# Optimization experiments

Measured on AMD Instinct MI355X. Metric: run time of the kernel, lower is better.

The kernel has to match this reference:

```python
import jax, jax.numpy as jnp
import numpy as np

B, N, D_MODEL, N_HEADS, WINDOW = 2, 2048, 1024, 16, 512
HEAD_DIM = D_MODEL // N_HEADS

def setup_inputs() -> dict:
    key = jax.random.key(0)
    k1, k2, k3 = jax.random.split(key, 3)
    x = jax.random.normal(k1, (B, N, D_MODEL), dtype=jnp.float32)
    W_qkv = jax.random.normal(k2, (D_MODEL, 3 * D_MODEL), dtype=jnp.float32) * 0.02
    W_proj = jax.random.normal(k3, (D_MODEL, D_MODEL), dtype=jnp.float32) * 0.02
    b_proj = jnp.zeros((D_MODEL,), dtype=jnp.float32)
    return {"x": x, "W_qkv": W_qkv, "W_proj": W_proj, "b_proj": b_proj}

def reference(x, W_qkv, W_proj, b_proj):
    Bx, Nx, C = x.shape
    H, Dh = N_HEADS, C // N_HEADS
    scale = Dh ** -0.5
    window = min(WINDOW, Nx)
    half = window // 2
    # qkv: [B,N,3C] -> [3,B,H,N,Dh]
    qkv = (x @ W_qkv).reshape(Bx, Nx, 3, H, Dh).transpose(2, 0, 3, 1, 4)
    q, k, v = qkv[0], qkv[1], qkv[2]
    # banded mask: allowed iff i-half <= j <= i+half
    i = jnp.arange(Nx)[:, None]
    j = jnp.arange(Nx)[None, :]
    allowed = jnp.abs(i - j) <= half  # [N,N] bool
    attn = jnp.einsum('bhqd,bhkd->bhqk', q, k) * scale
    attn = jnp.where(allowed[None, None], attn, -jnp.inf)
    attn = jax.nn.softmax(attn, axis=-1)
    out = jnp.einsum('bhqk,bhkd->bhqd', attn, v)
    out = out.transpose(0, 2, 1, 3).reshape(Bx, Nx, C)
    return out @ W_proj + b_proj
```

## Files before the change

kernel.cpp:

```cpp
#include <hip/hip_runtime.h>
#include <stdint.h>


typedef _Float16 f16x8 __attribute__((ext_vector_type(8)));
typedef _Float16 f16x4 __attribute__((ext_vector_type(4)));
typedef __fp16   fp16x2n __attribute__((ext_vector_type(2)));
typedef float    f32x4 __attribute__((ext_vector_type(4)));
typedef float    f32x16 __attribute__((ext_vector_type(16)));

#define MFMA16(a, b, c) __builtin_amdgcn_mfma_f32_16x16x32_f16((a), (b), (c), 0, 0, 0)
#define MFMA32(a, b, c) __builtin_amdgcn_mfma_f32_32x32x16_f16((a), (b), (c), 0, 0, 0)

__device__ __forceinline__ void gload16(const void* g, void* l) {
  __builtin_amdgcn_global_load_lds(
      (const __attribute__((address_space(1))) void*)g,
      (__attribute__((address_space(3))) void*)l, 16, 0, 0);
}

__device__ __forceinline__ unsigned pk2(float a, float b) {
  fp16x2n t = __builtin_amdgcn_cvt_pkrtz(a, b);
  return __builtin_bit_cast(unsigned, t);
}

__global__ __launch_bounds__(256) void prep(const float* __restrict__ x,
                                            const float* __restrict__ wqkv,
                                            const float* __restrict__ wproj,
                                            _Float16* __restrict__ Xb,
                                            _Float16* __restrict__ Wqt,
                                            _Float16* __restrict__ Wpt) {
  __shared__ float t[64][65];
  const int id = blockIdx.x, tid = threadIdx.x;
  if (id < 4096) {
    int i = (id * 256 + tid) * 4;
    float4 v = *(const float4*)(x + i);
    f16x4 h;
    h[0] = (_Float16)v.x; h[1] = (_Float16)v.y;
    h[2] = (_Float16)v.z; h[3] = (_Float16)v.w;
    *(f16x4*)(Xb + i) = h;
    return;
  }
  const float* in; _Float16* out; int N, bx, by;
  if (id < 4864) { int tt = id - 4096; in = wqkv; out = Wqt; N = 3072; bx = tt % 48; by = tt / 48; }
  else           { int tt = id - 4864; in = wproj; out = Wpt; N = 1024; bx = tt & 15; by = tt >> 4; }
  const int n0 = bx * 64, k0 = by * 64;
  {
    int j = tid & 63;
#pragma unroll
    for (int p = 0; p < 16; p++) {
      int i = p * 4 + (tid >> 6);
      t[i][j] = in[(size_t)(k0 + i) * N + n0 + j];
    }
  }
  __syncthreads();
  {
    int i = tid & 63;
#pragma unroll
    for (int p = 0; p < 16; p++) {
      int j = p * 4 + (tid >> 6);
      out[(size_t)(n0 + j) * 1024 + k0 + i] = (_Float16)t[i][j];
    }
  }
}

__global__ __launch_bounds__(256) void vtrans(const _Float16* __restrict__ V,
                                              _Float16* __restrict__ Vt) {
  __shared__ _Float16 t[64][66];
  const int tid = threadIdx.x;
  const int bh = blockIdx.y, n0 = blockIdx.x * 64;
  const _Float16* Vg = V + (size_t)bh * 131072;
  {
    int dh0 = (tid & 7) * 8;
#pragma unroll
    for (int p = 0; p < 2; p++) {
      int nl = p * 32 + (tid >> 3);
      f16x8 v = *(const f16x8*)(Vg + (size_t)(n0 + nl) * 64 + dh0);
#pragma unroll
      for (int e = 0; e < 8; e++) t[nl][dh0 + e] = v[e];
    }
  }
  __syncthreads();
  {
    int dh = tid >> 2, nb = (tid & 3) * 16;
    f16x8 a, b;
#pragma unroll
    for (int e = 0; e < 8; e++) { a[e] = t[nb + e][dh]; b[e] = t[nb + 8 + e][dh]; }
    _Float16* dst = Vt + (size_t)bh * 131072 + (size_t)dh * 2048 + n0 + nb;
    *(f16x8*)dst = a;
    *(f16x8*)(dst + 8) = b;
  }
}

template <int BM, int BN, int EPI>
__global__ __launch_bounds__(256) void gemm16(const _Float16* __restrict__ A,
                                              const _Float16* __restrict__ Bt,
                                              const int K,
                                              _Float16* __restrict__ oh,
                                              float* __restrict__ of,
                                              const float* __restrict__ bias,
                                              const int Nout) {
  constexpr int RF = BM / 32, CF = BN / 32;
  constexpr int SLABS = (BM + BN) / 8;
  __shared__ __align__(16) char smem[(BM + BN) * 128];
  char* As = smem;
  char* Bs = smem + BM * 128;
  const int tid = threadIdx.x, wave = tid >> 6, lane = tid & 63;
  const int il = lane & 15, ih = lane >> 4;
  const int bm = blockIdx.y * BM, bn = blockIdx.x * BN;
  const int wm = wave >> 1, wn = wave & 1;
  const int rs = lane >> 3, cp = lane & 7;

  f32x4 acc[RF][CF] = {};

  for (int k0 = 0; k0 < K; k0 += 64) {
    __syncthreads();
#pragma unroll
    for (int s0 = 0; s0 < SLABS / 4; s0++) {
      int s = wave + s0 * 4;
      int row = s * 8 + rs;
      int c = cp ^ (row & 7);
      if (row < BM)
        gload16(A + (size_t)(bm + row) * K + k0 + c * 8, As + s * 1024);
      else
        gload16(Bt + (size_t)(bn + row - BM) * K + k0 + c * 8, smem + s * 1024);
    }
    __syncthreads();
#pragma unroll
    for (int ks = 0; ks < 2; ks++) {
      f16x8 af[RF], bf[CF];
#pragma unroll
      for (int rf = 0; rf < RF; rf++) {
        int R = wm * (BM / 2) + rf * 16 + il;
        af[rf] = *(const f16x8*)(As + R * 128 + (((ks * 4 + ih) ^ (R & 7)) * 16));
      }
#pragma unroll
      for (int cf = 0; cf < CF; cf++) {
        int C = wn * (BN / 2) + cf * 16 + il;
        bf[cf] = *(const f16x8*)(Bs + C * 128 + (((ks * 4 + ih) ^ (C & 7)) * 16));
      }
#pragma unroll
      for (int rf = 0; rf < RF; rf++)
#pragma unroll
        for (int cf = 0; cf < CF; cf++)
          acc[rf][cf] = MFMA16(af[rf], bf[cf], acc[rf][cf]);
    }
  }

#pragma unroll
  for (int rf = 0; rf < RF; rf++)
#pragma unroll
    for (int cf = 0; cf < CF; cf++)
#pragma unroll
      for (int r = 0; r < 4; r++) {
        int row = bm + wm * (BM / 2) + rf * 16 + ih * 4 + r;
        int col = bn + wn * (BN / 2) + cf * 16 + il;
        float v = acc[rf][cf][r];
        if (EPI == 0) {
          int sec = col >> 10, cc = col & 1023;
          if (sec == 0) v *= 0.18033688f;
          size_t plane = (size_t)(sec * 32 + (row >> 11) * 16 + (cc >> 6));
          oh[plane * 131072 + (size_t)(row & 2047) * 64 + (cc & 63)] = (_Float16)v;
        } else {
          of[(size_t)row * Nout + col] = v + bias[col];
        }
      }
}

__global__ __launch_bounds__(512) void attn(const _Float16* __restrict__ QKV,
                                            const _Float16* __restrict__ VT,
                                            _Float16* __restrict__ O2) {
  __shared__ __align__(16) char smem[65536];
  char* Qs = smem;
  const int tid = threadIdx.x, wave = tid >> 6, lane = tid & 63;
  const int cl = lane & 31, hl = lane >> 5;
  const int rs = lane >> 3, cp = lane & 7;
  const int q0 = blockIdx.x * 256, bh = blockIdx.y;
  const _Float16* Qg = QKV + (size_t)bh * 131072;
  const _Float16* Kg = QKV + 4194304 + (size_t)bh * 131072;
  const _Float16* Vg = VT + (size_t)bh * 131072;
  const int t0 = (q0 >= 256) ? q0 - 256 : 0;
  const int t1 = (q0 + 512 <= 2048) ? q0 + 512 : 2048;
  const int niter = (t1 - t0) >> 6;

#pragma unroll
  for (int s0 = 0; s0 < 4; s0++) {
    int s = wave * 4 + s0;
    int row = s * 8 + rs;
    int c = cp ^ (row & 7);
    gload16(Qg + (size_t)(q0 + row) * 64 + c * 8, Qs + s * 1024);
  }
  {
    char* B0 = smem + 32768;
    int row = wave * 8 + rs;
    int c = cp ^ (row & 7);
    gload16(Kg + (size_t)(t0 + row) * 64 + c * 8, B0 + wave * 1024);
    gload16(Vg + (size_t)row * 2048 + t0 + c * 8, B0 + 8192 + wave * 1024);
  }
  __syncthreads();

  f16x8 bq[4];
  {
    int row = 32 * wave + cl;
#pragma unroll
    for (int ks = 0; ks < 4; ks++)
      bq[ks] = *(const f16x8*)(Qs + row * 128 + (((ks * 2 + hl) ^ (row & 7)) * 16));
  }

  f32x16 oacc[2] = {};
  float l_acc = 0.f;
  const int a0 = q0 + 32 * wave;

  for (int i = 0; i < niter; i++) {
    const int kt = t0 + i * 64;
    char* Bc = smem + 32768 + (i & 1) * 16384;
    if (i + 1 < niter) {
      char* Bn = smem + 32768 + ((i + 1) & 1) * 16384;
      int row = wave * 8 + rs;
      int c = cp ^ (row & 7);
      gload16(Kg + (size_t)(kt + 64 + row) * 64 + c * 8, Bn + wave * 1024);
      gload16(Vg + (size_t)row * 2048 + (kt + 64) + c * 8, Bn + 8192 + wave * 1024);
    }
    char* Ksm = Bc;
    char* Vsm = Bc + 8192;
#pragma unroll
    for (int cb = 0; cb < 2; cb++) {
      const int d0 = a0 - (kt + 32 * cb);
      if (d0 >= 288 || d0 <= -288) continue;
      f32x16 st = {};
#pragma unroll
      for (int ks = 0; ks < 4; ks++) {
        int krow = 32 * cb + cl;
        f16x8 ak = *(const f16x8*)(Ksm + krow * 128 + (((ks * 2 + hl) ^ (krow & 7)) * 16));
        st = MFMA32(ak, bq[ks], st);
      }
      uint32_t q4x[4], q4y[4];
#pragma unroll
      for (int g = 0; g < 4; g++) {
        float v[4];
#pragma unroll
        for (int i2 = 0; i2 < 4; i2++) {
          float e = __builtin_amdgcn_exp2f(st[4 * g + i2]);
          int kl = 8 * g + 4 * hl + i2;
          if (d0 == 256) e = (cl <= kl) ? e : 0.f;
          else if (d0 == -256) e = (cl >= kl) ? e : 0.f;
          l_acc += e;
          v[i2] = e;
        }
        q4x[g] = pk2(v[0], v[1]);
        q4y[g] = pk2(v[2], v[3]);
      }
#pragma unroll
      for (int ks2 = 0; ks2 < 2; ks2++) {
        uint32_t qax = q4x[2 * ks2], qay = q4y[2 * ks2];
        uint32_t qbx = q4x[2 * ks2 + 1], qby = q4y[2 * ks2 + 1];
        uint32_t rax = __shfl_xor(qax, 32), ray = __shfl_xor(qay, 32);
        uint32_t rbx = __shfl_xor(qbx, 32), rby = __shfl_xor(qby, 32);
        uint32_t lox = hl ? rbx : qax, loy = hl ? rby : qay;
        uint32_t hix = hl ? qbx : rax, hiy = hl ? qby : ray;
        union { uint32_t u[4]; f16x8 h; } bp;
        bp.u[0] = lox; bp.u[1] = loy; bp.u[2] = hix; bp.u[3] = hiy;
#pragma unroll
        for (int db = 0; db < 2; db++) {
          int vrow = 32 * db + cl;
          f16x8 av = *(const f16x8*)(Vsm + vrow * 128 +
                                     (((cb * 4 + ks2 * 2 + hl) ^ (vrow & 7)) * 16));
          oacc[db] = MFMA32(av, bp.h, oacc[db]);
        }
      }
    }
    __syncthreads();
  }

  l_acc += __shfl_xor(l_acc, 32);
  const float inv = 1.0f / l_acc;
  const int b = bh >> 4, h = bh & 15;
  _Float16* dst = O2 + (size_t)(b * 2048 + a0 + cl) * 1024 + h * 64;
#pragma unroll
  for (int db = 0; db < 2; db++)
#pragma unroll
    for (int g = 0; g < 4; g++) {
      uint32_t lo = pk2(oacc[db][4 * g + 0] * inv, oacc[db][4 * g + 1] * inv);
      uint32_t hi = pk2(oacc[db][4 * g + 2] * inv, oacc[db][4 * g + 3] * inv);
      uint2 pkd = {lo, hi};
      *(uint2*)(dst + 32 * db + 8 * g + 4 * hl) = pkd;
    }
}


extern "C" void kernel_launch(void* const* d_in, const int* in_sizes, int n_in,
                              void* d_out, int out_size, void* d_ws, size_t ws_size,
                              hipStream_t stream) {
  const float* x = (const float*)d_in[0];
  const float* wqkv = (const float*)d_in[1];
  const float* wproj = (const float*)d_in[2];
  const float* bproj = (const float*)d_in[3];
  float* out = (float*)d_out;
  char* ws = (char*)d_ws;

  _Float16* Xb  = (_Float16*)(ws);
  _Float16* Wqt = (_Float16*)(ws + (size_t)(8  << 20));
  _Float16* Wpt = (_Float16*)(ws + (size_t)(14 << 20));
  _Float16* QKV = (_Float16*)(ws + (size_t)(16 << 20));
  _Float16* Vt  = (_Float16*)(ws + (size_t)(40 << 20));
  _Float16* O2  = (_Float16*)(ws);

  prep<<<5120, 256, 0, stream>>>(x, wqkv, wproj, Xb, Wqt, Wpt);
  gemm16<128, 128, 0><<<dim3(24, 32), 256, 0, stream>>>(Xb, Wqt, 1024, QKV, nullptr,
                                                        nullptr, 0);
  vtrans<<<dim3(32, 32), 256, 0, stream>>>(QKV + 8388608, Vt);
  attn<<<dim3(8, 32), 512, 0, stream>>>(QKV, Vt, O2);
  gemm16<128, 64, 1><<<dim3(16, 32), 256, 0, stream>>>(O2, Wpt, 1024, nullptr, out,
                                                       bproj, 1024);
}
```

Baseline: 175.1 us.

## Split attention key tiles across wave pairs and merge partial outputs via LDS

```diff
diff --git a/kernel.cpp b/kernel.cpp
--- a/kernel.cpp
+++ b/kernel.cpp
@@ -5,6 +5,7 @@
 typedef _Float16 f16x8 __attribute__((ext_vector_type(8)));
 typedef _Float16 f16x4 __attribute__((ext_vector_type(4)));
 typedef __fp16   fp16x2n __attribute__((ext_vector_type(2)));
+typedef float    f32x2 __attribute__((ext_vector_type(2)));
 typedef float    f32x4 __attribute__((ext_vector_type(4)));
 typedef float    f32x16 __attribute__((ext_vector_type(16)));
 
@@ -168,28 +169,28 @@
 __global__ __launch_bounds__(512) void attn(const _Float16* __restrict__ QKV,
                                             const _Float16* __restrict__ VT,
                                             _Float16* __restrict__ O2) {
-  __shared__ __align__(16) char smem[65536];
-  char* Qs = smem;
+  __shared__ __align__(16) char smem[51200];
   const int tid = threadIdx.x, wave = tid >> 6, lane = tid & 63;
+  const int qw = wave >> 1, sh = wave & 1;
   const int cl = lane & 31, hl = lane >> 5;
   const int rs = lane >> 3, cp = lane & 7;
-  const int q0 = blockIdx.x * 256, bh = blockIdx.y;
+  const int q0 = blockIdx.x * 128, bh = blockIdx.y;
   const _Float16* Qg = QKV + (size_t)bh * 131072;
   const _Float16* Kg = QKV + 4194304 + (size_t)bh * 131072;
   const _Float16* Vg = VT + (size_t)bh * 131072;
   const int t0 = (q0 >= 256) ? q0 - 256 : 0;
-  const int t1 = (q0 + 512 <= 2048) ? q0 + 512 : 2048;
+  const int t1 = (q0 + 384 <= 2048) ? q0 + 384 : 2048;
   const int niter = (t1 - t0) >> 6;
 
 #pragma unroll
-  for (int s0 = 0; s0 < 4; s0++) {
-    int s = wave * 4 + s0;
+  for (int q = 0; q < 2; q++) {
+    int s = 2 * wave + q;
     int row = s * 8 + rs;
     int c = cp ^ (row & 7);
-    gload16(Qg + (size_t)(q0 + row) * 64 + c * 8, Qs + s * 1024);
-  }
-  {
-    char* B0 = smem + 32768;
+    gload16(Qg + (size_t)(q0 + row) * 64 + c * 8, smem + s * 1024);
+  }
+  {
+    char* B0 = smem + 18432;
     int row = wave * 8 + rs;
     int c = cp ^ (row & 7);
     gload16(Kg + (size_t)(t0 + row) * 64 + c * 8, B0 + wave * 1024);
@@ -199,40 +200,41 @@
 
   f16x8 bq[4];
   {
-    int row = 32 * wave + cl;
+    int row = 32 * qw + cl;
 #pragma unroll
     for (int ks = 0; ks < 4; ks++)
-      bq[ks] = *(const f16x8*)(Qs + row * 128 + (((ks * 2 + hl) ^ (row & 7)) * 16));
-  }
-
+      bq[ks] = *(const f16x8*)(smem + row * 128 + (((ks * 2 + hl) ^ (row & 7)) * 16));
+  }
+  __syncthreads();
+
+  char* Pw = smem + wave * 2304;
   f32x16 oacc[2] = {};
   float l_acc = 0.f;
-  const int a0 = q0 + 32 * wave;
+  const int a0 = q0 + 32 * qw;
 
   for (int i = 0; i < niter; i++) {
     const int kt = t0 + i * 64;
-    char* Bc = smem + 32768 + (i & 1) * 16384;
+    char* Bc = smem + 18432 + (i & 1) * 16384;
     if (i + 1 < niter) {
-      char* Bn = smem + 32768 + ((i + 1) & 1) * 16384;
+      char* Bn = smem + 18432 + ((i + 1) & 1) * 16384;
       int row = wave * 8 + rs;
       int c = cp ^ (row & 7);
       gload16(Kg + (size_t)(kt + 64 + row) * 64 + c * 8, Bn + wave * 1024);
       gload16(Vg + (size_t)row * 2048 + (kt + 64) + c * 8, Bn + 8192 + wave * 1024);
     }
-    char* Ksm = Bc;
-    char* Vsm = Bc + 8192;
-#pragma unroll
-    for (int cb = 0; cb < 2; cb++) {
-      const int d0 = a0 - (kt + 32 * cb);
-      if (d0 >= 288 || d0 <= -288) continue;
+    const int d0 = a0 - (kt + 32 * sh);
+    if (d0 < 288 && d0 > -288) {
+      char* Ksm = Bc;
+      char* Vsm = Bc + 8192;
       f32x16 st = {};
-#pragma unroll
-      for (int ks = 0; ks < 4; ks++) {
-        int krow = 32 * cb + cl;
-        f16x8 ak = *(const f16x8*)(Ksm + krow * 128 + (((ks * 2 + hl) ^ (krow & 7)) * 16));
-        st = MFMA32(ak, bq[ks], st);
-      }
-      uint32_t q4x[4], q4y[4];
+      {
+        const int krow = 32 * sh + cl;
+#pragma unroll
+        for (int ks = 0; ks < 4; ks++) {
+          f16x8 ak = *(const f16x8*)(Ksm + krow * 128 + (((ks * 2 + hl) ^ (krow & 7)) * 16));
+          st = MFMA32(ak, bq[ks], st);
+        }
+      }
 #pragma unroll
       for (int g = 0; g < 4; g++) {
         float v[4];
@@ -245,24 +247,19 @@
           l_acc += e;
           v[i2] = e;
         }
-        q4x[g] = pk2(v[0], v[1]);
-        q4y[g] = pk2(v[2], v[3]);
+        uint2 w2 = {pk2(v[0], v[1]), pk2(v[2], v[3])};
+        *(uint2*)(Pw + cl * 72 + 16 * g + 8 * hl) = w2;
       }
 #pragma unroll
       for (int ks2 = 0; ks2 < 2; ks2++) {
-        uint32_t qax = q4x[2 * ks2], qay = q4y[2 * ks2];
-        uint32_t qbx = q4x[2 * ks2 + 1], qby = q4y[2 * ks2 + 1];
-        uint32_t rax = __shfl_xor(qax, 32), ray = __shfl_xor(qay, 32);
-        uint32_t rbx = __shfl_xor(qbx, 32), rby = __shfl_xor(qby, 32);
-        uint32_t lox = hl ? rbx : qax, loy = hl ? rby : qay;
-        uint32_t hix = hl ? qbx : rax, hiy = hl ? qby : ray;
-        union { uint32_t u[4]; f16x8 h; } bp;
-        bp.u[0] = lox; bp.u[1] = loy; bp.u[2] = hix; bp.u[3] = hiy;
+        union { uint2 u2[2]; f16x8 h; } bp;
+        bp.u2[0] = *(const uint2*)(Pw + cl * 72 + 32 * ks2 + 16 * hl);
+        bp.u2[1] = *(const uint2*)(Pw + cl * 72 + 32 * ks2 + 16 * hl + 8);
 #pragma unroll
         for (int db = 0; db < 2; db++) {
           int vrow = 32 * db + cl;
           f16x8 av = *(const f16x8*)(Vsm + vrow * 128 +
-                                     (((cb * 4 + ks2 * 2 + hl) ^ (vrow & 7)) * 16));
+                                     (((4 * sh + 2 * ks2 + hl) ^ (vrow & 7)) * 16));
           oacc[db] = MFMA32(av, bp.h, oacc[db]);
         }
       }
@@ -270,19 +267,41 @@
     __syncthreads();
   }
 
-  l_acc += __shfl_xor(l_acc, 32);
-  const float inv = 1.0f / l_acc;
-  const int b = bh >> 4, h = bh & 15;
-  _Float16* dst = O2 + (size_t)(b * 2048 + a0 + cl) * 1024 + h * 64;
-#pragma unroll
-  for (int db = 0; db < 2; db++)
-#pragma unroll
-    for (int g = 0; g < 4; g++) {
-      uint32_t lo = pk2(oacc[db][4 * g + 0] * inv, oacc[db][4 * g + 1] * inv);
-      uint32_t hi = pk2(oacc[db][4 * g + 2] * inv, oacc[db][4 * g + 3] * inv);
-      uint2 pkd = {lo, hi};
-      *(uint2*)(dst + 32 * db + 8 * g + 4 * hl) = pkd;
-    }
+  const float lp = l_acc + __shfl_xor(l_acc, 32);
+  char* Mq = smem + qw * 8448;
+  if (sh == 1) {
+#pragma unroll
+    for (int db = 0; db < 2; db++)
+#pragma unroll
+      for (int g = 0; g < 4; g++) {
+        int dh0 = 32 * db + 8 * g + 4 * hl;
+        f32x2 a = {oacc[db][4 * g + 0], oacc[db][4 * g + 1]};
+        f32x2 b = {oacc[db][4 * g + 2], oacc[db][4 * g + 3]};
+        *(f32x2*)(Mq + cl * 264 + dh0 * 4) = a;
+        *(f32x2*)(Mq + cl * 264 + dh0 * 4 + 8) = b;
+      }
+    if (hl == 0) *(float*)(smem + 34816 + (qw * 32 + cl) * 4) = lp;
+  }
+  __syncthreads();
+  if (sh == 0) {
+    float lo = *(const float*)(smem + 34816 + (qw * 32 + cl) * 4);
+    float inv = 1.0f / (lp + lo);
+    const int b = bh >> 4, h = bh & 15;
+    _Float16* dst = O2 + (size_t)(b * 2048 + a0 + cl) * 1024 + h * 64;
+#pragma unroll
+    for (int db = 0; db < 2; db++)
+#pragma unroll
+      for (int g = 0; g < 4; g++) {
+        int dh0 = 32 * db + 8 * g + 4 * hl;
+        f32x2 a = *(const f32x2*)(Mq + cl * 264 + dh0 * 4);
+        f32x2 b2 = *(const f32x2*)(Mq + cl * 264 + dh0 * 4 + 8);
+        uint2 pkd = {pk2((oacc[db][4 * g + 0] + a[0]) * inv,
+                         (oacc[db][4 * g + 1] + a[1]) * inv),
+                     pk2((oacc[db][4 * g + 2] + b2[0]) * inv,
+                         (oacc[db][4 * g + 3] + b2[1]) * inv)};
+        *(uint2*)(dst + dh0) = pkd;
+      }
+  }
 }
 
 
@@ -307,7 +326,7 @@
   gemm16<128, 128, 0><<<dim3(24, 32), 256, 0, stream>>>(Xb, Wqt, 1024, QKV, nullptr,
                                                         nullptr, 0);
   vtrans<<<dim3(32, 32), 256, 0, stream>>>(QKV + 8388608, Vt);
-  attn<<<dim3(8, 32), 512, 0, stream>>>(QKV, Vt, O2);
+  attn<<<dim3(16, 32), 512, 0, stream>>>(QKV, Vt, O2);
   gemm16<128, 64, 1><<<dim3(16, 32), 256, 0, stream>>>(O2, Wpt, 1024, nullptr, out,
                                                        bproj, 1024);
 }
```

Result: faster. 160.9 us (-8.1%).
